# Optimization experiments

Hardware: AMD Instinct MI355X
Metric: run time of the kernel (lower is better)

The kernel has to match this reference:

```python
import jax, jax.numpy as jnp
import numpy as np

B, L, ENC, DEC, ATT = 64, 1024, 1024, 1024, 1024


def setup_inputs() -> dict:
    key = jax.random.key(0)
    ks = jax.random.split(key, 8)
    s1 = 1.0 / np.sqrt(ENC)
    s2 = 1.0 / np.sqrt(DEC)
    s3 = 1.0 / np.sqrt(ATT)
    return {
        "features": jax.random.normal(ks[0], (B, L, ENC), jnp.float32),
        "hidden_state": jax.random.normal(ks[1], (B, DEC), jnp.float32),
        "W1_w": jax.random.uniform(ks[2], (ENC, ATT), jnp.float32, -s1, s1),
        "W1_b": jax.random.uniform(ks[3], (ATT,), jnp.float32, -s1, s1),
        "W2_w": jax.random.uniform(ks[4], (DEC, ATT), jnp.float32, -s2, s2),
        "W2_b": jax.random.uniform(ks[5], (ATT,), jnp.float32, -s2, s2),
        "V_w": jax.random.uniform(ks[6], (ATT,), jnp.float32, -s3, s3),
        "V_b": jax.random.uniform(ks[7], (), jnp.float32, -s3, s3),
    }


def reference(features, hidden_state, W1_w, W1_b, W2_w, W2_b, V_w, V_b):
    # proj_f: [B, L, ATT]; proj_h: [B, 1, ATT]
    proj_f = jnp.einsum('ble,ea->bla', features, W1_w) + W1_b
    proj_h = (hidden_state @ W2_w + W2_b)[:, None, :]
    scores = jnp.tanh(proj_f + proj_h) @ V_w + V_b  # [B, L]
    alpha = jax.nn.softmax(scores, axis=1)
    context = jnp.einsum('bl,ble->be', alpha, features)
    return alpha, context
```

## Files before the change

### kernel.cpp

```cpp
#include <hip/hip_runtime.h>
#include <hip/hip_bf16.h>


typedef __bf16 bf16x8 __attribute__((ext_vector_type(8)));
typedef float floatx4 __attribute__((ext_vector_type(4)));
typedef unsigned short ushort_t;
typedef unsigned long long u64;

__device__ __forceinline__ ushort_t f2b(float x) {
    union { float f; unsigned u; } v; v.f = x;
    unsigned r = (v.u + 0x7fffu + ((v.u >> 16) & 1u)) >> 16;
    return (ushort_t)r;
}

__device__ __forceinline__ float b2f(ushort_t u) {
    union { unsigned u; float f; } v; v.u = (unsigned)u << 16; return v.f;
}

__device__ __forceinline__ u64 pack4(float4 f) {
    return (u64)f2b(f.x) | ((u64)f2b(f.y) << 16) |
           ((u64)f2b(f.z) << 32) | ((u64)f2b(f.w) << 48);
}

__device__ __forceinline__ void gload_lds16(const void* g, void* l) {
    __builtin_amdgcn_global_load_lds(
        (const __attribute__((address_space(1))) void*)g,
        (__attribute__((address_space(3))) void*)l, 16, 0, 0);
}

__device__ __forceinline__ float fast_tanh(float x) {
    const float ax = fabsf(x);
    const float t  = __expf(-2.0f * ax);
    const float r  = (1.0f - t) * __builtin_amdgcn_rcpf(1.0f + t);
    return copysignf(r, x);
}

#define LOG2E2 2.885390082f

__global__ __launch_bounds__(256) void convert_feat_kernel(
    const float* __restrict__ feat, ushort_t* __restrict__ featb) {
    const size_t idx = ((size_t)blockIdx.x * 256 + threadIdx.x) * 8;
    const float4 f0 = *(const float4*)(feat + idx);
    const float4 f1 = *(const float4*)(feat + idx + 4);
    *(u64*)(featb + idx)     = pack4(f0);
    *(u64*)(featb + idx + 4) = pack4(f1);
}

__global__ __launch_bounds__(256) void transpose_w1_kernel(
    const float* __restrict__ w1, ushort_t* __restrict__ w1t) {
    __shared__ ushort_t tile[64][65];
    const int k0 = blockIdx.x * 64, n0 = blockIdx.y * 64;
    const int tr = threadIdx.x >> 6;
    const int tc = threadIdx.x & 63;
#pragma unroll
    for (int i = 0; i < 16; i++) {
        int r = i * 4 + tr;
        tile[tc][r] = f2b(w1[(size_t)(k0 + r) * 1024 + n0 + tc]);
    }
    __syncthreads();
#pragma unroll
    for (int i = 0; i < 16; i++) {
        int r = i * 4 + tr;
        w1t[(size_t)(n0 + r) * 1024 + k0 + tc] = tile[r][tc];
    }
}

__global__ __launch_bounds__(256) void projh_kernel(
    const float* __restrict__ hidden, const float* __restrict__ w2,
    const float* __restrict__ w2b, const float* __restrict__ w1b,
    float* __restrict__ ph) {
    const int b  = blockIdx.y;
    const int al = threadIdx.x & 63;
    const int eg = threadIdx.x >> 6;
    const int a  = blockIdx.x * 64 + al;
    const float* h = hidden + b * 1024;
    float sum = 0.f;
    const int e0 = eg * 256;
#pragma unroll 8
    for (int e = e0; e < e0 + 256; e++)
        sum += h[e] * w2[(size_t)e * 1024 + a];
    __shared__ float red[256];
    red[threadIdx.x] = sum;
    __syncthreads();
    if (threadIdx.x < 64)
        ph[b * 1024 + a] = w2b[a] + w1b[a] + red[al] + red[al + 64] +
                           red[al + 128] + red[al + 192];
}


#define WAITV(n) asm volatile("s_waitcnt vmcnt(" #n ")" ::: "memory")
#define BAR() __builtin_amdgcn_s_barrier()

#define STG_A(d, h, kc) do { \
    gload_lds16(aSrc + (kc) + (h) * 32,          aDst + (d) * 16384 + (h) * 8192); \
    gload_lds16(aSrc + 131072 + (kc) + (h) * 32, aDst + (d) * 16384 + (h) * 8192 + 4096); \
  } while (0)
#define STG_B(d, h, kc) do { \
    gload_lds16(bSrc + (kc) + (h) * 32,          bDst + (d) * 16384 + (h) * 8192); \
    gload_lds16(bSrc + 131072 + (kc) + (h) * 32, bDst + (d) * 16384 + (h) * 8192 + 4096); \
  } while (0)

#define PHASE(d, h, mq, LOADB) do { \
    bf16x8 af[4]; \
    _Pragma("unroll") \
    for (int i_ = 0; i_ < 4; i_++) \
      af[i_] = *(const bf16x8*)(As + (d) * 16384 + (h) * 8192 + \
                                (ga + (mq) * 4 + i_) * 512 + rdo); \
    if (LOADB) { \
      _Pragma("unroll") \
      for (int j_ = 0; j_ < 4; j_++) \
        bf[j_] = *(const bf16x8*)(Bs + (d) * 16384 + (h) * 8192 + \
                                  (gb + j_) * 512 + rdo); \
    } \
    __builtin_amdgcn_s_setprio(1); \
    _Pragma("unroll") \
    for (int i_ = 0; i_ < 4; i_++) \
      _Pragma("unroll") \
      for (int j_ = 0; j_ < 4; j_++) \
        acc[(mq) * 4 + i_][j_] = __builtin_amdgcn_mfma_f32_16x16x32_bf16( \
            af[i_], bf[j_], acc[(mq) * 4 + i_][j_], 0, 0, 0); \
    __builtin_amdgcn_s_setprio(0); \
  } while (0)

#define TILE(t, d) do { \
    const int k1_ = (((t) + 1) & 15) * 64; \
    const int k2_ = (((t) + 2) & 15) * 64; \
    STG_A(d ^ 1, 1, k1_); \
    PHASE(d, 0, 0, 1); \
    STG_B(d ^ 1, 1, k1_); \
    PHASE(d, 0, 1, 0); \
    WAITV(8); BAR(); \
    STG_A(d, 0, k2_); \
    PHASE(d, 1, 0, 1); \
    STG_B(d, 0, k2_); \
    PHASE(d, 1, 1, 0); \
    WAITV(8); BAR(); \
  } while (0)

__global__ __launch_bounds__(512, 2) void gemm_scores_256_kernel(
    const ushort_t* __restrict__ featb,
    const ushort_t* __restrict__ w1t,
    const float* __restrict__ ph,
    const float* __restrict__ vw,
    float* __restrict__ part) {
    __shared__ ushort_t As[2 * 16384];
    __shared__ ushort_t Bs[2 * 16384];
    __shared__ float cbias[256];
    __shared__ float vvw[256];

    const int tid = threadIdx.x;
    const int orig = blockIdx.x;
    const int wgid = (orig & 7) * 128 + (orig >> 3);
    const int nt = wgid & 3;
    const int mt = wgid >> 2;
    const int n0 = nt * 256;
    const int m0 = mt * 256;
    const int b  = m0 >> 10;

    if (tid < 256) {
        cbias[tid] = ph[(b << 10) + n0 + tid];
        vvw[tid]   = vw[n0 + tid];
    }

    const int w    = tid >> 6;
    const int lane = tid & 63;
    const int q    = lane >> 4;
    const int l15  = lane & 15;
    const int rdo  = l15 * 32 + ((q ^ ((l15 >> 1) & 3)) << 3);
    const int ga   = (w >> 2) * 8;
    const int gb   = (w & 3) * 4;
    const int sb   = ((lane & 3) ^ ((lane >> 3) & 3)) << 3;

    const ushort_t* aSrc = featb + (size_t)(m0 + w * 16 + (lane >> 2)) * 1024 + sb;
    const ushort_t* bSrc = w1t  + (size_t)(n0 + w * 16 + (lane >> 2)) * 1024 + sb;
    ushort_t* aDst = As + w * 512;
    ushort_t* bDst = Bs + w * 512;

    floatx4 acc[8][4] = {};
    bf16x8 bf[4];

    STG_A(0, 0, 0);  STG_B(0, 0, 0);
    STG_A(0, 1, 0);  STG_B(0, 1, 0);
    STG_A(1, 0, 64); STG_B(1, 0, 64);
    WAITV(8); BAR();

    for (int it = 0; it < 8; it++) {
        TILE(2 * it,     0);
        TILE(2 * it + 1, 1);
    }
    WAITV(0);

    float vv[4], cbk[4];
    float sum_vvw = 0.f;
#pragma unroll
    for (int j = 0; j < 4; j++) {
        const int col = (w & 3) * 64 + j * 16 + l15;
        vv[j]  = vvw[col];
        cbk[j] = LOG2E2 * cbias[col];
        sum_vvw += vv[j];
    }
    const int slot  = nt * 4 + (w & 3);
    const int rbase = m0 + (w >> 2) * 128;
#pragma unroll
    for (int mf = 0; mf < 8; mf++) {
#pragma unroll
        for (int r = 0; r < 4; r++) {
            const int row = rbase + mf * 16 + q * 4 + r;
            float s2 = 0.f;
#pragma unroll
            for (int j = 0; j < 4; j++) {
                const float arg = fmaf(LOG2E2, acc[mf][j][r], cbk[j]);
                const float e   = __builtin_amdgcn_exp2f(arg);
                s2 = fmaf(__builtin_amdgcn_rcpf(1.0f + e), vv[j], s2);
            }
            float s = fmaf(-2.0f, s2, sum_vvw);
            s += __shfl_xor(s, 1);
            s += __shfl_xor(s, 2);
            s += __shfl_xor(s, 4);
            s += __shfl_xor(s, 8);
            if (l15 == 0) part[slot * 65536 + row] = s;
        }
    }
}

__global__ __launch_bounds__(256) void softmax_kernel(
    const float* __restrict__ part, float* __restrict__ alpha) {
    const int b = blockIdx.x;
    const int tid = threadIdx.x;
    __shared__ float red[256];
    float v[4];
    float mx = -1e30f;
#pragma unroll
    for (int i = 0; i < 4; i++) {
        const int m = b * 1024 + tid + i * 256;
        float s = 0.f;
#pragma unroll
        for (int nb = 0; nb < 16; nb++) s += part[nb * 65536 + m];
        v[i] = s;
        mx = fmaxf(mx, s);
    }
    red[tid] = mx; __syncthreads();
    for (int s = 128; s > 0; s >>= 1) {
        if (tid < s) red[tid] = fmaxf(red[tid], red[tid + s]);
        __syncthreads();
    }
    mx = red[0]; __syncthreads();
    float sum = 0.f;
#pragma unroll
    for (int i = 0; i < 4; i++) { v[i] = __expf(v[i] - mx); sum += v[i]; }
    red[tid] = sum; __syncthreads();
    for (int s = 128; s > 0; s >>= 1) {
        if (tid < s) red[tid] += red[tid + s];
        __syncthreads();
    }
    const float inv = 1.0f / red[0];
#pragma unroll
    for (int i = 0; i < 4; i++)
        alpha[b * 1024 + tid + i * 256] = v[i] * inv;
}

__global__ __launch_bounds__(1024) void context_bf16_kernel(
    const float* __restrict__ alpha, const ushort_t* __restrict__ featb,
    float* __restrict__ ctx) {
    const int b  = blockIdx.y;
    const int el = threadIdx.x & 63;
    const int lg = threadIdx.x >> 6;
    const int e  = blockIdx.x * 256 + el * 4;
    const ushort_t* fb = featb + ((size_t)b << 20) + e;
    const float* ab = alpha + b * 1024;
    floatx4 acc = {};
    const int l0 = lg * 64;
#pragma unroll 4
    for (int l = l0; l < l0 + 64; l++) {
        const float a = ab[l];
        const ushort4 u = *(const ushort4*)(fb + (size_t)l * 1024);
        acc[0] = fmaf(a, b2f(u.x), acc[0]);
        acc[1] = fmaf(a, b2f(u.y), acc[1]);
        acc[2] = fmaf(a, b2f(u.z), acc[2]);
        acc[3] = fmaf(a, b2f(u.w), acc[3]);
    }
    __shared__ floatx4 red[16 * 64];
    red[lg * 64 + el] = acc;
    __syncthreads();
#pragma unroll
    for (int s = 8; s > 0; s >>= 1) {
        if (lg < s) red[lg * 64 + el] += red[(lg + s) * 64 + el];
        __syncthreads();
    }
    if (lg == 0)
        *(floatx4*)(ctx + b * 1024 + e) = red[el];
}

__global__ __launch_bounds__(1024) void context_kernel(
    const float* __restrict__ alpha, const float* __restrict__ feat,
    float* __restrict__ ctx) {
    const int b  = blockIdx.y;
    const int el = threadIdx.x & 63;
    const int lg = threadIdx.x >> 6;
    const int e  = blockIdx.x * 256 + el * 4;
    const float* fb = feat + (size_t)b * 1024 * 1024;
    const float* ab = alpha + b * 1024;
    floatx4 acc = {};
    const int l0 = lg * 64;
#pragma unroll 4
    for (int l = l0; l < l0 + 64; l++) {
        const float a = ab[l];
        const floatx4 f = *(const floatx4*)(fb + (size_t)l * 1024 + e);
        acc += a * f;
    }
    __shared__ floatx4 red[16 * 64];
    red[lg * 64 + el] = acc;
    __syncthreads();
#pragma unroll
    for (int s = 8; s > 0; s >>= 1) {
        if (lg < s) red[lg * 64 + el] += red[(lg + s) * 64 + el];
        __syncthreads();
    }
    if (lg == 0)
        *(floatx4*)(ctx + b * 1024 + e) = red[el];
}

#define KP 72
__global__ __launch_bounds__(256) void gemm_scores_f32_kernel(
    const float* __restrict__ feat, const ushort_t* __restrict__ w1t,
    const float* __restrict__ ph, const float* __restrict__ vw,
    float* __restrict__ part) {
    __shared__ ushort_t Asf[128 * KP];
    __shared__ ushort_t Bsf[128 * KP];
    __shared__ float cbias[128];
    __shared__ float vvw[128];
    const int tid = threadIdx.x;
    const int nt = blockIdx.x, n0 = nt * 128, m0 = blockIdx.y * 128;
    const int b = m0 >> 10;
    if (tid < 128) { cbias[tid] = ph[(b << 10) + n0 + tid]; vvw[tid] = vw[n0 + tid]; }
    const int wave = tid >> 6, lane = tid & 63;
    const int wr = (wave >> 1) * 64, wc = (wave & 1) * 64;
    const int q = lane >> 4, l15 = lane & 15;
    floatx4 acc[4][4] = {};
    const int arow = tid >> 4, acol = (tid & 15) * 4;
    const int brow = tid >> 3, bcol = (tid & 7) * 8;
    const float* aptr = feat + (size_t)m0 * 1024;
    const ushort_t* bptr = w1t + (size_t)n0 * 1024;
    for (int kt = 0; kt < 1024; kt += 64) {
#pragma unroll
        for (int p = 0; p < 8; p++) {
            int r = p * 16 + arow;
            const float4 f = *(const float4*)(aptr + (size_t)r * 1024 + kt + acol);
            *(u64*)&Asf[r * KP + acol] = pack4(f);
        }
#pragma unroll
        for (int p = 0; p < 4; p++) {
            int r = p * 32 + brow;
            *(uint4*)&Bsf[r * KP + bcol] =
                *(const uint4*)(bptr + (size_t)r * 1024 + kt + bcol);
        }
        __syncthreads();
#pragma unroll
        for (int ks = 0; ks < 64; ks += 32) {
            bf16x8 af[4], bfr[4];
#pragma unroll
            for (int t = 0; t < 4; t++)
                af[t] = *(const bf16x8*)&Asf[(wr + t * 16 + l15) * KP + ks + q * 8];
#pragma unroll
            for (int t = 0; t < 4; t++)
                bfr[t] = *(const bf16x8*)&Bsf[(wc + t * 16 + l15) * KP + ks + q * 8];
#pragma unroll
            for (int tm = 0; tm < 4; tm++)
#pragma unroll
                for (int tn = 0; tn < 4; tn++)
                    acc[tm][tn] = __builtin_amdgcn_mfma_f32_16x16x32_bf16(
                        af[tm], bfr[tn], acc[tm][tn], 0, 0, 0);
        }
        __syncthreads();
    }
    const int slot = nt * 2 + (wave & 1);
#pragma unroll
    for (int tm = 0; tm < 4; tm++) {
#pragma unroll
        for (int r = 0; r < 4; r++) {
            const int row = wr + tm * 16 + q * 4 + r;
            float s = 0.f;
#pragma unroll
            for (int tn = 0; tn < 4; tn++) {
                const int col = wc + tn * 16 + l15;
                s += fast_tanh(acc[tm][tn][r] + cbias[col]) * vvw[col];
            }
            s += __shfl_xor(s, 1);
            s += __shfl_xor(s, 2);
            s += __shfl_xor(s, 4);
            s += __shfl_xor(s, 8);
            if (l15 == 0) part[slot * 65536 + m0 + row] = s;
        }
    }
}

extern "C" void kernel_launch(void* const* d_in, const int* in_sizes, int n_in,
                              void* d_out, int out_size, void* d_ws, size_t ws_size,
                              hipStream_t stream) {
    const float* feat = (const float*)d_in[0];
    const float* hid  = (const float*)d_in[1];
    const float* w1w  = (const float*)d_in[2];
    const float* w1b  = (const float*)d_in[3];
    const float* w2w  = (const float*)d_in[4];
    const float* w2b  = (const float*)d_in[5];
    const float* vw   = (const float*)d_in[6];

    const size_t FEATB_BYTES = (size_t)64 * 1024 * 1024 * 2;
    const size_t W1T_BYTES   = (size_t)1024 * 1024 * 2;
    const size_t PH_BYTES    = (size_t)64 * 1024 * 4;
    const size_t PART_BYTES  = (size_t)16 * 65536 * 4;
    const bool   big_ws = ws_size >= FEATB_BYTES + W1T_BYTES + PH_BYTES + PART_BYTES;
    if (!big_ws && ws_size < W1T_BYTES + PH_BYTES + PART_BYTES) return;

    char* ws = (char*)d_ws;
    ushort_t* featb = (ushort_t*)ws;
    size_t off = big_ws ? FEATB_BYTES : 0;
    ushort_t* w1t  = (ushort_t*)(ws + off);
    float* ph      = (float*)(ws + off + W1T_BYTES);
    float* part    = (float*)(ws + off + W1T_BYTES + PH_BYTES);

    float* alpha = (float*)d_out;
    float* ctx   = alpha + 64 * 1024;

    transpose_w1_kernel<<<dim3(16, 16), 256, 0, stream>>>(w1w, w1t);
    projh_kernel<<<dim3(16, 64), 256, 0, stream>>>(hid, w2w, w2b, w1b, ph);
    if (big_ws) {
        convert_feat_kernel<<<32768, 256, 0, stream>>>(feat, featb);
        gemm_scores_256_kernel<<<dim3(1024), 512, 0, stream>>>(
            featb, w1t, ph, vw, part);
        softmax_kernel<<<64, 256, 0, stream>>>(part, alpha);
        context_bf16_kernel<<<dim3(4, 64), 1024, 0, stream>>>(alpha, featb, ctx);
    } else {
        gemm_scores_f32_kernel<<<dim3(8, 512), 256, 0, stream>>>(
            feat, w1t, ph, vw, part);
        softmax_kernel<<<64, 256, 0, stream>>>(part, alpha);
        context_kernel<<<dim3(4, 64), 1024, 0, stream>>>(alpha, feat, ctx);
    }
}
```

Baseline: 577.4 us.

## Fuse fp32-to-bf16 feature conversion into the scores GEMM A-tile loader

```diff
diff --git a/kernel.cpp b/kernel.cpp
--- a/kernel.cpp
+++ b/kernel.cpp
@@ -36,15 +36,6 @@
 }
 
 #define LOG2E2 2.885390082f
-
-__global__ __launch_bounds__(256) void convert_feat_kernel(
-    const float* __restrict__ feat, ushort_t* __restrict__ featb) {
-    const size_t idx = ((size_t)blockIdx.x * 256 + threadIdx.x) * 8;
-    const float4 f0 = *(const float4*)(feat + idx);
-    const float4 f1 = *(const float4*)(feat + idx + 4);
-    *(u64*)(featb + idx)     = pack4(f0);
-    *(u64*)(featb + idx + 4) = pack4(f1);
-}
 
 __global__ __launch_bounds__(256) void transpose_w1_kernel(
     const float* __restrict__ w1, ushort_t* __restrict__ w1t) {
@@ -91,25 +82,50 @@
 #define WAITV(n) asm volatile("s_waitcnt vmcnt(" #n ")" ::: "memory")
 #define BAR() __builtin_amdgcn_s_barrier()
 
-#define STG_A(d, h, kc) do { \
-    gload_lds16(aSrc + (kc) + (h) * 32,          aDst + (d) * 16384 + (h) * 8192); \
-    gload_lds16(aSrc + 131072 + (kc) + (h) * 32, aDst + (d) * 16384 + (h) * 8192 + 4096); \
-  } while (0)
 #define STG_B(d, h, kc) do { \
     gload_lds16(bSrc + (kc) + (h) * 32,          bDst + (d) * 16384 + (h) * 8192); \
     gload_lds16(bSrc + 131072 + (kc) + (h) * 32, bDst + (d) * 16384 + (h) * 8192 + 4096); \
   } while (0)
 
-#define PHASE(d, h, mq, LOADB) do { \
+#define LDA_F4(tt) do { \
+    const int kc_ = ((tt) & 15) * 64; \
+    _Pragma("unroll") \
+    for (int u_ = 0; u_ < 4; u_++) { \
+        const int h_ = u_ >> 1, rb_ = u_ & 1; \
+        const float* p_ = aSrcF + rb_ * 131072 + kc_ + h_ * 32; \
+        fA[u_ * 2]     = *(const float4*)(p_); \
+        fA[u_ * 2 + 1] = *(const float4*)(p_ + 4); \
+    } } while (0)
+
+#define WRA(dd, tt) do { \
+    const int sel_ = (((tt) >> 2) == nt); \
+    const int kc_  = ((tt) & 15) * 64; \
+    _Pragma("unroll") \
+    for (int u_ = 0; u_ < 4; u_++) { \
+        const int h_ = u_ >> 1, rb_ = u_ & 1; \
+        const u64 lo_ = pack4(fA[u_ * 2]); \
+        const u64 hi_ = pack4(fA[u_ * 2 + 1]); \
+        u64* ld_ = (u64*)(As + (dd) * 16384 + h_ * 8192 + rb_ * 4096 + \
+                          w * 512 + lane * 8); \
+        ld_[0] = lo_; ld_[1] = hi_; \
+        if (sel_) { \
+            u64* g_ = (u64*)(featbO + \
+                (size_t)(m0 + w * 16 + rb_ * 128 + (lane >> 2)) * 1024 + \
+                kc_ + h_ * 32 + sbe); \
+            g_[0] = lo_; g_[1] = hi_; \
+        } \
+    } } while (0)
+
+#define CBLK(dd, h, mq, LB) do { \
     bf16x8 af[4]; \
     _Pragma("unroll") \
     for (int i_ = 0; i_ < 4; i_++) \
-      af[i_] = *(const bf16x8*)(As + (d) * 16384 + (h) * 8192 + \
+      af[i_] = *(const bf16x8*)(As + (dd) * 16384 + (h) * 8192 + \
                                 (ga + (mq) * 4 + i_) * 512 + rdo); \
-    if (LOADB) { \
+    if (LB) { \
       _Pragma("unroll") \
       for (int j_ = 0; j_ < 4; j_++) \
-        bf[j_] = *(const bf16x8*)(Bs + (d) * 16384 + (h) * 8192 + \
+        bf[j_] = *(const bf16x8*)(Bs + (dd) * 16384 + (h) * 8192 + \
                                   (gb + j_) * 512 + rdo); \
     } \
     __builtin_amdgcn_s_setprio(1); \
@@ -122,27 +138,18 @@
     __builtin_amdgcn_s_setprio(0); \
   } while (0)
 
-#define TILE(t, d) do { \
-    const int k1_ = (((t) + 1) & 15) * 64; \
-    const int k2_ = (((t) + 2) & 15) * 64; \
-    STG_A(d ^ 1, 1, k1_); \
-    PHASE(d, 0, 0, 1); \
-    STG_B(d ^ 1, 1, k1_); \
-    PHASE(d, 0, 1, 0); \
-    WAITV(8); BAR(); \
-    STG_A(d, 0, k2_); \
-    PHASE(d, 1, 0, 1); \
-    STG_B(d, 0, k2_); \
-    PHASE(d, 1, 1, 0); \
-    WAITV(8); BAR(); \
+#define COMPUTE(dd) do { \
+    CBLK(dd, 0, 0, 1); CBLK(dd, 0, 1, 0); \
+    CBLK(dd, 1, 0, 1); CBLK(dd, 1, 1, 0); \
   } while (0)
 
-__global__ __launch_bounds__(512, 2) void gemm_scores_256_kernel(
-    const ushort_t* __restrict__ featb,
+__global__ __launch_bounds__(512, 2) void gemm_scores_fused_kernel(
+    const float* __restrict__ feat,
     const ushort_t* __restrict__ w1t,
     const float* __restrict__ ph,
     const float* __restrict__ vw,
-    float* __restrict__ part) {
+    float* __restrict__ part,
+    ushort_t* __restrict__ featbO) {
     __shared__ ushort_t As[2 * 16384];
     __shared__ ushort_t Bs[2 * 16384];
     __shared__ float cbias[256];
@@ -169,24 +176,36 @@
     const int rdo  = l15 * 32 + ((q ^ ((l15 >> 1) & 3)) << 3);
     const int ga   = (w >> 2) * 8;
     const int gb   = (w & 3) * 4;
-    const int sb   = ((lane & 3) ^ ((lane >> 3) & 3)) << 3;
-
-    const ushort_t* aSrc = featb + (size_t)(m0 + w * 16 + (lane >> 2)) * 1024 + sb;
-    const ushort_t* bSrc = w1t  + (size_t)(n0 + w * 16 + (lane >> 2)) * 1024 + sb;
-    ushort_t* aDst = As + w * 512;
+    const int sbe  = ((lane & 3) ^ ((lane >> 3) & 3)) << 3;
+
+    const float*    aSrcF = feat + (size_t)(m0 + w * 16 + (lane >> 2)) * 1024 + sbe;
+    const ushort_t* bSrc  = w1t  + (size_t)(n0 + w * 16 + (lane >> 2)) * 1024 + sbe;
     ushort_t* bDst = Bs + w * 512;
 
     floatx4 acc[8][4] = {};
     bf16x8 bf[4];
-
-    STG_A(0, 0, 0);  STG_B(0, 0, 0);
-    STG_A(0, 1, 0);  STG_B(0, 1, 0);
-    STG_A(1, 0, 64); STG_B(1, 0, 64);
-    WAITV(8); BAR();
-
-    for (int it = 0; it < 8; it++) {
-        TILE(2 * it,     0);
-        TILE(2 * it + 1, 1);
+    float4 fA[8];
+
+    LDA_F4(0);
+    STG_B(0, 0, 0); STG_B(0, 1, 0);
+    WAITV(4);
+    WRA(0, 0);
+    LDA_F4(1);
+    WAITV(8);
+    asm volatile("s_waitcnt lgkmcnt(0)" ::: "memory");
+    BAR();
+
+    for (int t = 0; t < 16; t++) {
+        const int d  = t & 1;
+        const int k1 = ((t + 1) & 15) * 64;
+        STG_B(d ^ 1, 0, k1); STG_B(d ^ 1, 1, k1);
+        COMPUTE(d);
+        WAITV(4);
+        WRA(d ^ 1, t + 1);
+        LDA_F4(t + 2);
+        WAITV(8);
+        asm volatile("s_waitcnt lgkmcnt(0)" ::: "memory");
+        BAR();
     }
     WAITV(0);
 
@@ -425,9 +444,8 @@
     transpose_w1_kernel<<<dim3(16, 16), 256, 0, stream>>>(w1w, w1t);
     projh_kernel<<<dim3(16, 64), 256, 0, stream>>>(hid, w2w, w2b, w1b, ph);
     if (big_ws) {
-        convert_feat_kernel<<<32768, 256, 0, stream>>>(feat, featb);
-        gemm_scores_256_kernel<<<dim3(1024), 512, 0, stream>>>(
-            featb, w1t, ph, vw, part);
+        gemm_scores_fused_kernel<<<dim3(1024), 512, 0, stream>>>(
+            feat, w1t, ph, vw, part, featb);
         softmax_kernel<<<64, 256, 0, stream>>>(part, alpha);
         context_bf16_kernel<<<dim3(4, 64), 1024, 0, stream>>>(alpha, featb, ctx);
     } else {
```

Result: no change. 585.3 us (+1.4%).
